# Kernel optimization log

Hardware: AMD Instinct MI355X
Metric: run time of the kernel (lower is better)

The kernel has to match this reference:

```python
import jax, jax.numpy as jnp
from jax import lax
import numpy as np

B, S, T, R = 64, 50, 50, 2   # batch, n_prev_sents, n_words, n_responses
V, H = 32000, 256            # vocab, hidden (= emb_size)


def gru_scan(xs, h0, Wih, Whh, bih, bhh):
    """Torch-style GRU over xs [T, N, I]; returns (outs [T,N,H], h_last [N,H])."""
    gi_all = jnp.einsum('tni,gi->tng', xs, Wih) + bih  # input gates precomputed
    def step(h, gi):
        gh = h @ Whh.T + bhh
        ir, iz, inn = jnp.split(gi, 3, -1)
        hr, hz, hn = jnp.split(gh, 3, -1)
        r = jax.nn.sigmoid(ir + hr)
        z = jax.nn.sigmoid(iz + hz)
        n = jnp.tanh(inn + r * hn)
        h = (1.0 - z) * n + z * h
        return h, h
    h_last, outs = lax.scan(step, h0, gi_all)
    return outs, h_last


def agent_tables():
    # replicates get_agent_emb: np.random.seed(1), one fresh uniform table per batch
    np.random.seed(1)
    return jnp.asarray(np.stack([np.random.uniform(0, 1, (S + 1, H)) for _ in range(B)]).astype(np.float32))


def setup_inputs() -> dict:
    key = jax.random.key(0)
    ks = jax.random.split(key, 24)
    k = 1.0 / np.sqrt(H)
    u = lambda kk, shape: jax.random.uniform(kk, shape, jnp.float32, -k, k)
    inp = {
        'context': jax.random.randint(ks[0], (B, S, T), 0, V, jnp.int32),
        'response': jax.random.randint(ks[1], (B, R, T), 0, V, jnp.int32),
        'spk_agents': jax.random.randint(ks[2], (B, S), 0, S + 1, jnp.int32),
        'emb_utter': jax.random.normal(ks[3], (V, H), jnp.float32) * 0.1,
        'emb_resp': jax.random.normal(ks[4], (V, H), jnp.float32) * 0.1,
        'utter_Wih': u(ks[5], (3 * H, H)), 'utter_Whh': u(ks[6], (3 * H, H)),
        'utter_bih': u(ks[7], (3 * H,)), 'utter_bhh': u(ks[8], (3 * H,)),
        'ctx_Wih': u(ks[9], (3 * H, 2 * H)), 'ctx_Whh': u(ks[10], (3 * H, H)),
        'ctx_bih': u(ks[11], (3 * H,)), 'ctx_bhh': u(ks[12], (3 * H,)),
        'resp_Wih': u(ks[13], (3 * H, H)), 'resp_Whh': u(ks[14], (3 * H, H)),
        'resp_bih': u(ks[15], (3 * H,)), 'resp_bhh': u(ks[16], (3 * H,)),
        'spk_Wih': u(ks[17], (3 * H, H)), 'spk_Whh': u(ks[18], (3 * H, H)),
        'spk_bih': u(ks[19], (3 * H,)), 'spk_bhh': u(ks[20], (3 * H,)),
    }
    return inp


def forward(context, response, spk_agents, emb_utter, emb_resp,
            utter_Wih, utter_Whh, utter_bih, utter_bhh,
            ctx_Wih, ctx_Whh, ctx_bih, ctx_bhh,
            resp_Wih, resp_Whh, resp_bih, resp_bhh,
            spk_Wih, spk_Whh, spk_bih, spk_bhh):
    # ---- utterance encoder: all B*S utterances batched through one GRU ----
    xu = emb_utter[context.reshape(B * S, T)]                 # [B*S, T, H]
    xu = jnp.transpose(xu, (1, 0, 2))                         # [T, B*S, H]
    _, hu = gru_scan(xu, jnp.zeros((B * S, H), jnp.float32),
                     utter_Wih, utter_Whh, utter_bih, utter_bhh)
    utter_hidden = hu.reshape(B, S, H).transpose(1, 0, 2)     # [S, B, H]

    # ---- agent embeddings (per-batch random tables, gathered by speaker id) ----
    tables = agent_tables()                                   # [B, S+1, H] constant
    agent_emb = jnp.take_along_axis(tables, spk_agents[:, :, None].astype(jnp.int32), axis=1)  # [B,S,H]
    agent_emb = jnp.transpose(agent_emb, (1, 0, 2))           # [S, B, H]

    # ---- context GRU over utterances ----
    ctx_in = jnp.concatenate([utter_hidden, agent_emb], axis=2)  # [S, B, 2H]
    context_output, ctx_h = gru_scan(ctx_in, jnp.zeros((B, H), jnp.float32),
                                     ctx_Wih, ctx_Whh, ctx_bih, ctx_bhh)
    context_hidden = ctx_h[None]                              # [1, B, H]

    # ---- speaker encoder: masked GRU == GRU over each speaker's subsequence ----
    sp_ids = jnp.arange(S + 1)
    active = (spk_agents[:, :, None] == sp_ids[None, None, :])  # [B, S, S+1]
    active_t = jnp.transpose(active, (1, 0, 2))                 # [S, B, S+1]
    gi_all = jnp.einsum('sbh,gh->sbg', context_output, spk_Wih) + spk_bih  # [S, B, 3H]

    def spk_step(h, inputs):
        gi, act = inputs                                        # gi [B,3H], act [B,S+1]
        gh = jnp.einsum('bsh,gh->bsg', h, spk_Whh) + spk_bhh    # [B, S+1, 3H]
        ir, iz, inn = jnp.split(gi[:, None, :], 3, -1)
        hr, hz, hn = jnp.split(gh, 3, -1)
        r = jax.nn.sigmoid(ir + hr)
        z = jax.nn.sigmoid(iz + hz)
        n = jnp.tanh(inn + r * hn)
        h_new = (1.0 - z) * n + z * h
        return jnp.where(act[:, :, None], h_new, h), None

    h_spk, _ = lax.scan(spk_step, jnp.zeros((B, S + 1, H), jnp.float32), (gi_all, active_t))
    present = active.any(axis=1)                               # [B, S+1]
    spk_emb = h_spk * present[:, :, None]                      # rows of absent speakers stay 0
    spk_emb_mask = (present & (sp_ids[None, :] > 0)).astype(jnp.float32)  # [B, S+1]

    # ---- response encoder: all B*R responses batched ----
    xr = emb_resp[response.reshape(B * R, T)]                  # [B*R, T, H]
    xr = jnp.transpose(xr, (1, 0, 2))                          # [T, B*R, H]
    outs, hr_ = gru_scan(xr, jnp.zeros((B * R, H), jnp.float32),
                         resp_Wih, resp_Whh, resp_bih, resp_bhh)
    resp_output = outs.reshape(T, B, R, H).transpose(2, 0, 1, 3)  # [R, T, B, H]
    resp_hidden = hr_.reshape(B, R, H).transpose(1, 0, 2)         # [R, B, H]

    return (context_output, context_hidden, resp_output, resp_hidden, spk_emb, spk_emb_mask)


def reference(context, response, spk_agents, emb_utter, emb_resp,
              utter_Wih, utter_Whh, utter_bih, utter_bhh,
              ctx_Wih, ctx_Whh, ctx_bih, ctx_bhh,
              resp_Wih, resp_Whh, resp_bih, resp_bhh,
              spk_Wih, spk_Whh, spk_bih, spk_bhh):
    return forward(context, response, spk_agents, emb_utter, emb_resp,
                   utter_Wih, utter_Whh, utter_bih, utter_bhh,
                   ctx_Wih, ctx_Whh, ctx_bih, ctx_bhh,
                   resp_Wih, resp_Whh, resp_bih, resp_bhh,
                   spk_Wih, spk_Whh, spk_bih, spk_bhh)
```

## Files before the change

kernel.cpp:

```cpp
#include <hip/hip_runtime.h>
#include <hip/hip_bf16.h>
#include <stdint.h>
#include <stdlib.h>
#include <math.h>

typedef __hip_bfloat16 bf16;
typedef unsigned short ushort;
typedef __attribute__((ext_vector_type(8))) short bhalf8;
typedef __attribute__((ext_vector_type(4))) float f32x4;

#define Bn 64
#define Sn 50
#define Tn 50
#define Hn 256

#define OFF_CTX_OUT   0
#define OFF_CTX_HID   819200
#define OFF_RESP_OUT  835584
#define OFF_RESP_HID  2473984
#define OFF_SPK_EMB   2506752
#define OFF_SPK_MASK  3342336

#define WS_FLAG   0u
#define WS_HU     256u
// ... 23 lines not shown
template<bool BF>
__device__ __forceinline__ bhalf8 ldfrag(const void* __restrict__ p, size_t i) {
    if (BF) {
        return *(const bhalf8*)((const ushort*)p + i);
    } else {
        const float* q = (const float*)p + i;
        float4 a = *(const float4*)q;
        float4 b = *(const float4*)(q + 4);
        bhalf8 r;
        r[0] = (short)f2bf(a.x); r[1] = (short)f2bf(a.y);
        r[2] = (short)f2bf(a.z); r[3] = (short)f2bf(a.w);
        r[4] = (short)f2bf(b.x); r[5] = (short)f2bf(b.y);
        r[6] = (short)f2bf(b.z); r[7] = (short)f2bf(b.w);
        return r;
    }
}
template<bool BF>
__device__ __forceinline__ float ldw(const void* __restrict__ p, int i) {
    return BF ? bf2f(((const ushort*)p)[i]) : ((const float*)p)[i];
}
template<bool BF>
__device__ __forceinline__ void stout(void* __restrict__ out, size_t i, float v) {
    if (BF) ((ushort*)out)[i] = f2bf(v);
    else    ((float*)out)[i] = v;
}
__device__ __forceinline__ float fsigm(float x) {
    return __builtin_amdgcn_rcpf(1.f + __expf(-x));
}
__device__ __forceinline__ float ftanh(float x) {
    float e = __expf(-2.f * x);
    return (1.f - e) * __builtin_amdgcn_rcpf(1.f + e);
}

__global__ void sniff_kernel(const void* __restrict__ w, int* __restrict__ flag) {
    const unsigned int* p = (const unsigned int*)w;
    int tid = threadIdx.x;
    bool big = false;
    for (int i = tid; i < 512; i += 64) {
        float v = b2f_bits(p[i] << 16);
        if (!(fabsf(v) <= 1.0f)) big = true;
    }
    unsigned long long m = __ballot(big);
    if (tid == 0) *flag = (m == 0ull) ? 1 : 0;
}


template<bool BF>
__device__ void vocab_utt_body(
    const void* __restrict__ emb_u, const void* __restrict__ uWih,
    const void* __restrict__ ubih,
    char* __restrict__ Q, float* __restrict__ SC,
    float* bhs, float (*rmx)[16])
{
    const int tid = threadIdx.x;
    const int w = tid >> 6, l = tid & 63, quad = l >> 4, c = l & 15;

    for (int i = tid; i < 768; i += 512) bhs[i] = ldw<BF>(ubih, i);

    bhalf8 wf[3][2][8];
    #pragma unroll
    for (int g = 0; g < 3; ++g)
        #pragma unroll
        for (int ctl = 0; ctl < 2; ++ctl) {
            const int gcol = g * 256 + 32 * w + 16 * ctl + c;
            #pragma unroll
            for (int tk = 0; tk < 8; ++tk)
                wf[g][ctl][tk] = ldfrag<BF>(uWih, (size_t)gcol * 256 + 32 * tk + 8 * quad);
        }
    __syncthreads();

    for (int vt = blockIdx.x; vt < 2000; vt += gridDim.x) {
        f32x4 acc[3][2];
        #pragma unroll
        for (int g = 0; g < 3; ++g)
            #pragma unroll
            for (int ctl = 0; ctl < 2; ++ctl) {
                float b = bhs[g * 256 + 32 * w + 16 * ctl + c];
                acc[g][ctl] = (f32x4){b, b, b, b};
            }
        #pragma unroll
        for (int tk = 0; tk < 8; ++tk) {
            bhalf8 a = ldfrag<BF>(emb_u, (size_t)(vt * 16 + c) * 256 + 32 * tk + 8 * quad);
            #pragma unroll
            for (int g = 0; g < 3; ++g)
                #pragma unroll
                for (int ctl = 0; ctl < 2; ++ctl)
                    acc[g][ctl] = __builtin_amdgcn_mfma_f32_16x16x32_bf16(
                        a, wf[g][ctl][tk], acc[g][ctl], 0, 0, 0);
        }

        float mx[4];
        #pragma unroll
        for (int r = 0; r < 4; ++r) {
            float v = 0.f;
            #pragma unroll
            for (int g = 0; g < 3; ++g)
                #pragma unroll
                for (int ctl = 0; ctl < 2; ++ctl)
                    v = fmaxf(v, fabsf(acc[g][ctl][r]));
            mx[r] = v;
        }
        #pragma unroll
        for (int off = 1; off < 16; off <<= 1)
            #pragma unroll
            for (int r = 0; r < 4; ++r)
                mx[r] = fmaxf(mx[r], __shfl_xor(mx[r], off));
        if (c == 0)
            #pragma unroll
            for (int r = 0; r < 4; ++r) rmx[w][4 * quad + r] = mx[r];
        __syncthreads();

        #pragma unroll
        for (int r = 0; r < 4; ++r) {
            const int m = 4 * quad + r;
            float s = fmaxf(fmaxf(fmaxf(rmx[0][m], rmx[1][m]), fmaxf(rmx[2][m], rmx[3][m])),
                            fmaxf(fmaxf(rmx[4][m], rmx[5][m]), fmaxf(rmx[6][m], rmx[7][m])));
            float scale = s * (1.f / 127.f);
            float inv   = (s > 0.f) ? (127.f / s) : 0.f;
            #pragma unroll
            for (int g = 0; g < 3; ++g)
                #pragma unroll
                for (int ctl = 0; ctl < 2; ++ctl) {
                    int qv = __float2int_rn(acc[g][ctl][r] * inv);
                    qv = max(-127, min(127, qv));
                    Q[(size_t)(vt * 16 + m) * 768 + g * 256 + 32 * w + 16 * ctl + c] = (char)qv;
                }
            if (w == 0 && c == 0) SC[vt * 16 + m] = scale;
        }
        __syncthreads();
    }
}

__global__ __launch_bounds__(512, 1) void vocab_utt_kernel(
    const void* emb_u, const void* uWih, const void* ubih,
    char* Q, float* SC, const int* flag)
{
    __shared__ float bhs[768];
    __shared__ float rmx[8][16];
    if (*flag) vocab_utt_body<true >(emb_u, uWih, ubih, Q, SC, bhs, rmx);
    else       vocab_utt_body<false>(emb_u, uWih, ubih, Q, SC, bhs, rmx);
}

template<bool BF>
__device__ void rec_utt_body(
    const int* __restrict__ ctx_tok,
    const char* __restrict__ Q, const float* __restrict__ SC,
    const void* __restrict__ uWhh, const void* __restrict__ ubhh,
    ushort* __restrict__ H_u,
    char (*gq)[16][784], float* gsc_all , ushort (*hb)[16][264])
{
    const int n0 = blockIdx.x * 16;
    const int tid = threadIdx.x;
    const int w = tid >> 6, l = tid & 63, quad = l >> 4, c = l & 15;

    for (int i = tid; i < 16 * 264; i += 512) (&hb[0][0][0])[i] = 0;
    for (int i = tid; i < Tn * 16; i += 512) {
        const int t = i >> 4, m = i & 15;
        gsc_all[i] = SC[ctx_tok[(n0 + m) * Tn + t]];
    }

    float breg[3][2];
    #pragma unroll
    for (int g = 0; g < 3; ++g)
        #pragma unroll
        for (int ctl = 0; ctl < 2; ++ctl)
            breg[g][ctl] = ldw<BF>(ubhh, g * 256 + 32 * w + 16 * ctl + c);

    bhalf8 wf[3][2][8];
    #pragma unroll
    for (int g = 0; g < 3; ++g)
        #pragma unroll
        for (int ctl = 0; ctl < 2; ++ctl) {
            const int gcol = g * 256 + 32 * w + 16 * ctl + c;
            #pragma unroll
            for (int tk = 0; tk < 8; ++tk)
                wf[g][ctl][tk] = ldfrag<BF>(uWhh, (size_t)gcol * 256 + 32 * tk + 8 * quad);
        }

    float st[2][4];
    #pragma unroll
    for (int ctl = 0; ctl < 2; ++ctl)
        #pragma unroll
        for (int r = 0; r < 4; ++r) st[ctl][r] = 0.f;

    #pragma unroll
    for (int k = 0; k < 2; ++k) {
        const int m = 2 * w + k;
        const int tok = ctx_tok[(n0 + m) * Tn + 0];
        if (l < 48)
            gld_lds16(Q + (size_t)tok * 768 + l * 16, &gq[0][m][0]);
    }
    __syncthreads();

    int p = 0;
    for (int t = 0; t < Tn; ++t) {
        if (t < Tn - 1) {
            #pragma unroll
            for (int k = 0; k < 2; ++k) {
                const int m = 2 * w + k;
                const int tok = ctx_tok[(n0 + m) * Tn + t + 1];
                if (l < 48)
                    gld_lds16(Q + (size_t)tok * 768 + l * 16, &gq[p ^ 1][m][0]);
            }
        }

        f32x4 acc[3][2];
        #pragma unroll
        for (int g = 0; g < 3; ++g)
            #pragma unroll
            for (int ctl = 0; ctl < 2; ++ctl) {
                float b = breg[g][ctl];
                acc[g][ctl] = (f32x4){b, b, b, b};
            }
        #pragma unroll
        for (int tk = 0; tk < 8; ++tk) {
            bhalf8 a = *(const bhalf8*)(&hb[p][c][32 * tk + 8 * quad]);
            #pragma unroll
            for (int g = 0; g < 3; ++g)
                #pragma unroll
                for (int ctl = 0; ctl < 2; ++ctl)
                    acc[g][ctl] = __builtin_amdgcn_mfma_f32_16x16x32_bf16(
                        a, wf[g][ctl][tk], acc[g][ctl], 0, 0, 0);
        }

        #pragma unroll
        for (int ctl = 0; ctl < 2; ++ctl) {
            const int u = 32 * w + 16 * ctl + c;
            #pragma unroll
            for (int r = 0; r < 4; ++r) {
                const int m = 4 * quad + r;
                const float s = gsc_all[t * 16 + m];
                float gr = s * (float)(signed char)gq[p][m][u];
                float gz = s * (float)(signed char)gq[p][m][256 + u];
                float gn = s * (float)(signed char)gq[p][m][512 + u];
                float rr = fsigm(gr + acc[0][ctl][r]);
                float zz = fsigm(gz + acc[1][ctl][r]);
                float nn = ftanh(gn + rr * acc[2][ctl][r]);
                float h  = (1.f - zz) * nn + zz * st[ctl][r];
                st[ctl][r] = h;
                hb[p ^ 1][m][u] = f2bf(h);
            }
        }
        __syncthreads();
        p ^= 1;
    }

    #pragma unroll
    for (int ctl = 0; ctl < 2; ++ctl)
        #pragma unroll
        for (int r = 0; r < 4; ++r)
            H_u[(size_t)(n0 + 4 * quad + r) * Hn + 32 * w + 16 * ctl + c] = f2bf(st[ctl][r]);
}

__global__ __launch_bounds__(512, 1) void rec_utt_kernel(
    const int* ctx_tok, const char* Q, const float* SC,
    const void* uWhh, const void* ubhh, ushort* H_u, const int* flag)
{
    __shared__ __align__(16) char   gq[2][16][784];
    __shared__ float  gsc_all[Tn * 16];
    __shared__ __align__(16) ushort hb[2][16][264];
    if (*flag) rec_utt_body<true >(ctx_tok, Q, SC, uWhh, ubhh, H_u, gq, gsc_all, hb);
    else       rec_utt_body<false>(ctx_tok, Q, SC, uWhh, ubhh, H_u, gq, gsc_all, hb);
}

template<bool BF>
__device__ void respgi_body(
    int bid,
    const int* __restrict__ rsp_tok, const void* __restrict__ emb_r,
    const void* __restrict__ rWih, const void* __restrict__ rbih,
    ushort* __restrict__ RG, float* bhs)
{
    const int tid = threadIdx.x;
    const int w = tid >> 6, l = tid & 63, quad = l >> 4, c = l & 15;

    for (int i = tid; i < 768; i += 512) bhs[i] = ldw<BF>(rbih, i);

    bhalf8 wf[3][2][8];
    #pragma unroll
    for (int g = 0; g < 3; ++g)
        #pragma unroll
        for (int ctl = 0; ctl < 2; ++ctl) {
            const int gcol = g * 256 + 32 * w + 16 * ctl + c;
            #pragma unroll
            for (int tk = 0; tk < 8; ++tk)
                wf[g][ctl][tk] = ldfrag<BF>(rWih, (size_t)gcol * 256 + 32 * tk + 8 * quad);
        }
    __syncthreads();

    const int inst = bid * 16 + c;
    const int tok  = rsp_tok[inst];

    f32x4 acc[3][2];
    #pragma unroll
    for (int g = 0; g < 3; ++g)
        #pragma unroll
        for (int ctl = 0; ctl < 2; ++ctl) {
            float b = bhs[g * 256 + 32 * w + 16 * ctl + c];
            acc[g][ctl] = (f32x4){b, b, b, b};
        }
    #pragma unroll
    for (int tk = 0; tk < 8; ++tk) {
        bhalf8 a = ldfrag<BF>(emb_r, (size_t)tok * 256 + 32 * tk + 8 * quad);
        #pragma unroll
        for (int g = 0; g < 3; ++g)
            #pragma unroll
            for (int ctl = 0; ctl < 2; ++ctl)
                acc[g][ctl] = __builtin_amdgcn_mfma_f32_16x16x32_bf16(
                    a, wf[g][ctl][tk], acc[g][ctl], 0, 0, 0);
    }
    #pragma unroll
    for (int g = 0; g < 3; ++g)
        #pragma unroll
        for (int ctl = 0; ctl < 2; ++ctl)
            #pragma unroll
            for (int r = 0; r < 4; ++r)
                RG[(size_t)(bid * 16 + 4 * quad + r) * 768
                   + g * 256 + 32 * w + 16 * ctl + c] = f2bf(acc[g][ctl][r]);
}

template<bool BF>
__device__ void rec_resp_body(
    int bid,
    const ushort* __restrict__ RG,
    const void* __restrict__ rWhh, const void* __restrict__ rbhh,
    void* __restrict__ outp,
    ushort (*gx)[16][776], ushort (*hb)[16][264])
{
    const int n0 = bid * 16;
    const int tid = threadIdx.x;
    const int w = tid >> 6, l = tid & 63, quad = l >> 4, c = l & 15;

    for (int i = tid; i < 16 * 264; i += 512) (&hb[0][0][0])[i] = 0;

    float breg[3][2];
    #pragma unroll
    for (int g = 0; g < 3; ++g)
        #pragma unroll
        for (int ctl = 0; ctl < 2; ++ctl)
            breg[g][ctl] = ldw<BF>(rbhh, g * 256 + 32 * w + 16 * ctl + c);

    bhalf8 wf[3][2][8];
    #pragma unroll
    for (int g = 0; g < 3; ++g)
        #pragma unroll
        for (int ctl = 0; ctl < 2; ++ctl) {
            const int gcol = g * 256 + 32 * w + 16 * ctl + c;
            #pragma unroll
            for (int tk = 0; tk < 8; ++tk)
                wf[g][ctl][tk] = ldfrag<BF>(rWhh, (size_t)gcol * 256 + 32 * tk + 8 * quad);
        }

    float st[2][4];
    #pragma unroll
    for (int ctl = 0; ctl < 2; ++ctl)
        #pragma unroll
        for (int r = 0; r < 4; ++r) st[ctl][r] = 0.f;

    #pragma unroll
    for (int k = 0; k < 2; ++k) {
        const int m = 2 * w + k;
        const ushort* src = RG + (size_t)((n0 + m) * Tn + 0) * 768;
        if (l < 48) {
            gld_lds16(src + l * 8,       &gx[0][m][0]);
            gld_lds16(src + 384 + l * 8, &gx[0][m][384]);
        }
    }
    __syncthreads();

    int p = 0;
    for (int t = 0; t < Tn; ++t) {
        if (t < Tn - 1) {
            #pragma unroll
            for (int k = 0; k < 2; ++k) {
                const int m = 2 * w + k;
                const ushort* src = RG + (size_t)((n0 + m) * Tn + t + 1) * 768;
                if (l < 48) {
                    gld_lds16(src + l * 8,       &gx[p ^ 1][m][0]);
                    gld_lds16(src + 384 + l * 8, &gx[p ^ 1][m][384]);
                }
            }
        }
        if (t > 0) {
            #pragma unroll
            for (int ctl = 0; ctl < 2; ++ctl) {
                const int u = 32 * w + 16 * ctl + c;
                #pragma unroll
                for (int r = 0; r < 4; ++r) {
                    const int n = n0 + 4 * quad + r, bb = n >> 1, ri = n & 1;
                    stout<BF>(outp, OFF_RESP_OUT
                              + (size_t)((ri * Tn + (t - 1)) * Bn + bb) * Hn + u,
                              st[ctl][r]);
                }
            }
        }

        f32x4 acc[3][2];
        #pragma unroll
        for (int g = 0; g < 3; ++g)
            #pragma unroll
            for (int ctl = 0; ctl < 2; ++ctl) {
                float b = breg[g][ctl];
                acc[g][ctl] = (f32x4){b, b, b, b};
            }
        #pragma unroll
        for (int tk = 0; tk < 8; ++tk) {
            bhalf8 a = *(const bhalf8*)(&hb[p][c][32 * tk + 8 * quad]);
            #pragma unroll
            for (int g = 0; g < 3; ++g)
                #pragma unroll
                for (int ctl = 0; ctl < 2; ++ctl)
                    acc[g][ctl] = __builtin_amdgcn_mfma_f32_16x16x32_bf16(
                        a, wf[g][ctl][tk], acc[g][ctl], 0, 0, 0);
        }

        #pragma unroll
        for (int ctl = 0; ctl < 2; ++ctl) {
            const int u = 32 * w + 16 * ctl + c;
            #pragma unroll
            for (int r = 0; r < 4; ++r) {
                const int m = 4 * quad + r;
                float gr = bf2f(gx[p][m][u]);
                float gz = bf2f(gx[p][m][256 + u]);
                float gn = bf2f(gx[p][m][512 + u]);
                float rr = fsigm(gr + acc[0][ctl][r]);
                float zz = fsigm(gz + acc[1][ctl][r]);
                float nn = ftanh(gn + rr * acc[2][ctl][r]);
                float h  = (1.f - zz) * nn + zz * st[ctl][r];
                st[ctl][r] = h;
                hb[p ^ 1][m][u] = f2bf(h);
            }
        }
        __syncthreads();
        p ^= 1;
    }

    #pragma unroll
    for (int ctl = 0; ctl < 2; ++ctl) {
        const int u = 32 * w + 16 * ctl + c;
        #pragma unroll
        for (int r = 0; r < 4; ++r) {
            const int n = n0 + 4 * quad + r, bb = n >> 1, ri = n & 1;
            stout<BF>(outp, OFF_RESP_OUT
                      + (size_t)((ri * Tn + (Tn - 1)) * Bn + bb) * Hn + u, st[ctl][r]);
            stout<BF>(outp, OFF_RESP_HID + (size_t)(ri * Bn + bb) * Hn + u, st[ctl][r]);
        }
    }
}

template<bool BF>
__device__ void gi_ctx_body(
    int bid,
    const ushort* __restrict__ H_u, const ushort* __restrict__ tblbf,
    const int* __restrict__ spk_agents,
    const void* __restrict__ Wih, const void* __restrict__ bih,
    ushort* __restrict__ GIc, float* bhs)
{
    const int tid = threadIdx.x;
    const int w = tid >> 6, l = tid & 63, quad = l >> 4, c = l & 15;

    for (int i = tid; i < 768; i += 512) bhs[i] = ldw<BF>(bih, i);
    __syncthreads();

    const int m0 = bid * 16;
    const int m  = m0 + c, s = m >> 6, b = m & 63;
    const int a  = spk_agents[b * Sn + s];
    const ushort* arow0 = H_u   + (size_t)(b * Sn + s) * Hn;
    const ushort* arow1 = tblbf + (size_t)(b * 51 + a) * Hn;

    f32x4 acc[3][2];
    #pragma unroll
    for (int g = 0; g < 3; ++g)
        #pragma unroll
        for (int ctl = 0; ctl < 2; ++ctl) {
            float bb = bhs[g * 256 + 32 * w + 16 * ctl + c];
            acc[g][ctl] = (f32x4){bb, bb, bb, bb};
        }

    for (int half = 0; half < 2; ++half) {
        const ushort* ar = half ? arow1 : arow0;
        bhalf8 af[8];
        #pragma unroll
        for (int tk = 0; tk < 8; ++tk)
            af[tk] = *(const bhalf8*)(ar + 32 * tk + 8 * quad);
        #pragma unroll
        for (int g = 0; g < 3; ++g) {
            bhalf8 wf[2][8];
            #pragma unroll
            for (int ctl = 0; ctl < 2; ++ctl) {
                const int gcol = g * 256 + 32 * w + 16 * ctl + c;
                #pragma unroll
                for (int tk = 0; tk < 8; ++tk)
                    wf[ctl][tk] = ldfrag<BF>(Wih,
                        (size_t)gcol * 512 + half * 256 + 32 * tk + 8 * quad);
            }
            #pragma unroll
            for (int tk = 0; tk < 8; ++tk)
                #pragma unroll
                for (int ctl = 0; ctl < 2; ++ctl)
                    acc[g][ctl] = __builtin_amdgcn_mfma_f32_16x16x32_bf16(
                        af[tk], wf[ctl][tk], acc[g][ctl], 0, 0, 0);
        }
    }

    #pragma unroll
    for (int g = 0; g < 3; ++g)
        #pragma unroll
        for (int ctl = 0; ctl < 2; ++ctl)
            #pragma unroll
            for (int r = 0; r < 4; ++r)
                GIc[(size_t)(m0 + 4 * quad + r) * 768
                    + g * 256 + 32 * w + 16 * ctl + c] = f2bf(acc[g][ctl][r]);
}

__global__ __launch_bounds__(512, 1) void gates2_kernel(
    const int* rsp_tok, const void* emb_r, const void* rWih, const void* rbih,
    ushort* RG,
    const ushort* H_u, const ushort* tblbf, const int* spk_agents,
    const void* cWih, const void* cbih, ushort* GIc, const int* flag)
{
    __shared__ float bhs[768];
    if (blockIdx.x < 400) {
        if (*flag) respgi_body<true >(blockIdx.x, rsp_tok, emb_r, rWih, rbih, RG, bhs);
        else       respgi_body<false>(blockIdx.x, rsp_tok, emb_r, rWih, rbih, RG, bhs);
    } else {
        const int bid = blockIdx.x - 400;
        if (*flag) gi_ctx_body<true >(bid, H_u, tblbf, spk_agents, cWih, cbih, GIc, bhs);
        else       gi_ctx_body<false>(bid, H_u, tblbf, spk_agents, cWih, cbih, GIc, bhs);
    }
}

template<bool BF>
__device__ void ctx_rec_body(
    int bid,
    const ushort* __restrict__ GIc,
    const void* __restrict__ Whh, const void* __restrict__ bhh,
    float* __restrict__ CO, void* __restrict__ outp,
    ushort (*gx)[16][776], ushort (*hb)[16][264])
{
    const int n0 = bid * 16;
    const int tid = threadIdx.x;
    const int w = tid >> 6, l = tid & 63, quad = l >> 4, c = l & 15;

    for (int i = tid; i < 16 * 264; i += 512) (&hb[0][0][0])[i] = 0;

    float breg[3][2];
    #pragma unroll
    for (int g = 0; g < 3; ++g)
        #pragma unroll
        for (int ctl = 0; ctl < 2; ++ctl)
            breg[g][ctl] = ldw<BF>(bhh, g * 256 + 32 * w + 16 * ctl + c);

    bhalf8 wf[3][2][8];
    #pragma unroll
    for (int g = 0; g < 3; ++g)
        #pragma unroll
        for (int ctl = 0; ctl < 2; ++ctl) {
            const int gcol = g * 256 + 32 * w + 16 * ctl + c;
            #pragma unroll
            for (int tk = 0; tk < 8; ++tk)
                wf[g][ctl][tk] = ldfrag<BF>(Whh, (size_t)gcol * 256 + 32 * tk + 8 * quad);
        }

    float st[2][4];
    #pragma unroll
    for (int ctl = 0; ctl < 2; ++ctl)
        #pragma unroll
        for (int r = 0; r < 4; ++r) st[ctl][r] = 0.f;

    #pragma unroll
    for (int k = 0; k < 2; ++k) {
        const int m = 2 * w + k;
        const ushort* src = GIc + (size_t)(0 * Bn + n0 + m) * 768;
        if (l < 48) {
            gld_lds16(src + l * 8,       &gx[0][m][0]);
            gld_lds16(src + 384 + l * 8, &gx[0][m][384]);
        }
    }
    __syncthreads();

    int p = 0;
    for (int t = 0; t < Sn; ++t) {
        if (t < Sn - 1) {
            #pragma unroll
            for (int k = 0; k < 2; ++k) {
                const int m = 2 * w + k;
                const ushort* src = GIc + (size_t)((t + 1) * Bn + n0 + m) * 768;
                if (l < 48) {
                    gld_lds16(src + l * 8,       &gx[p ^ 1][m][0]);
                    gld_lds16(src + 384 + l * 8, &gx[p ^ 1][m][384]);
                }
            }
        }
        if (t > 0) {
            #pragma unroll
            for (int ctl = 0; ctl < 2; ++ctl) {
                const int u = 32 * w + 16 * ctl + c;
                #pragma unroll
                for (int r = 0; r < 4; ++r) {
                    const size_t gri = (size_t)((t - 1) * Bn + n0 + 4 * quad + r);
                    CO[gri * Hn + u] = st[ctl][r];
                    stout<BF>(outp, OFF_CTX_OUT + gri * Hn + u, st[ctl][r]);
                }
            }
        }

        f32x4 acc[3][2];
        #pragma unroll
        for (int g = 0; g < 3; ++g)
            #pragma unroll
            for (int ctl = 0; ctl < 2; ++ctl) {
                float b = breg[g][ctl];
                acc[g][ctl] = (f32x4){b, b, b, b};
            }
        #pragma unroll
        for (int tk = 0; tk < 8; ++tk) {
            bhalf8 a = *(const bhalf8*)(&hb[p][c][32 * tk + 8 * quad]);
            #pragma unroll
            for (int g = 0; g < 3; ++g)
                #pragma unroll
                for (int ctl = 0; ctl < 2; ++ctl)
                    acc[g][ctl] = __builtin_amdgcn_mfma_f32_16x16x32_bf16(
                        a, wf[g][ctl][tk], acc[g][ctl], 0, 0, 0);
        }

        #pragma unroll
        for (int ctl = 0; ctl < 2; ++ctl) {
            const int u = 32 * w + 16 * ctl + c;
            #pragma unroll
            for (int r = 0; r < 4; ++r) {
                const int m = 4 * quad + r;
                float gr = bf2f(gx[p][m][u]);
                float gz = bf2f(gx[p][m][256 + u]);
                float gn = bf2f(gx[p][m][512 + u]);
                float rr = fsigm(gr + acc[0][ctl][r]);
                float zz = fsigm(gz + acc[1][ctl][r]);
                float nn = ftanh(gn + rr * acc[2][ctl][r]);
                float h  = (1.f - zz) * nn + zz * st[ctl][r];
                st[ctl][r] = h;
                hb[p ^ 1][m][u] = f2bf(h);
            }
        }
        __syncthreads();
        p ^= 1;
    }

    #pragma unroll
    for (int ctl = 0; ctl < 2; ++ctl) {
        const int u = 32 * w + 16 * ctl + c;
        #pragma unroll
        for (int r = 0; r < 4; ++r) {
            const int m = 4 * quad + r;
            const size_t gri = (size_t)((Sn - 1) * Bn + n0 + m);
            CO[gri * Hn + u] = st[ctl][r];
            stout<BF>(outp, OFF_CTX_OUT + gri * Hn + u, st[ctl][r]);
            stout<BF>(outp, OFF_CTX_HID + (size_t)(n0 + m) * Hn + u, st[ctl][r]);
        }
    }
}

__global__ __launch_bounds__(512, 1) void rec2_kernel(
    const ushort* GIc, const void* cWhh, const void* cbhh, float* CO,
    const ushort* RG, const void* rWhh, const void* rbhh,
    void* outp, const int* flag)
{
    __shared__ __align__(16) ushort gx[2][16][776];
    __shared__ __align__(16) ushort hb[2][16][264];
    if (blockIdx.x < 4) {
        if (*flag) ctx_rec_body<true >(blockIdx.x, GIc, cWhh, cbhh, CO, outp, gx, hb);
        else       ctx_rec_body<false>(blockIdx.x, GIc, cWhh, cbhh, CO, outp, gx, hb);
    } else {
        const int bid = blockIdx.x - 4;
        if (*flag) rec_resp_body<true >(bid, RG, rWhh, rbhh, outp, gx, hb);
        else       rec_resp_body<false>(bid, RG, rWhh, rbhh, outp, gx, hb);
    }
}

template<bool BF>
__device__ void gi_spk_body(
    const float* __restrict__ CO,
    const void* __restrict__ Wih, const void* __restrict__ bih,
    ushort* __restrict__ GIs, float* bhs)
{
    const int tid = threadIdx.x;
    const int w = tid >> 6, l = tid & 63, quad = l >> 4, c = l & 15;

    for (int i = tid; i < 768; i += 512) bhs[i] = ldw<BF>(bih, i);

    bhalf8 wf[3][2][8];
    #pragma unroll
    for (int g = 0; g < 3; ++g)
        #pragma unroll
        for (int ctl = 0; ctl < 2; ++ctl) {
            const int gcol = g * 256 + 32 * w + 16 * ctl + c;
            #pragma unroll
            for (int tk = 0; tk < 8; ++tk)
                wf[g][ctl][tk] = ldfrag<BF>(Wih, (size_t)gcol * 256 + 32 * tk + 8 * quad);
        }
    __syncthreads();

    f32x4 acc[3][2];
    #pragma unroll
    for (int g = 0; g < 3; ++g)
        #pragma unroll
        for (int ctl = 0; ctl < 2; ++ctl) {
            float b = bhs[g * 256 + 32 * w + 16 * ctl + c];
            acc[g][ctl] = (f32x4){b, b, b, b};
        }
    #pragma unroll
    for (int tk = 0; tk < 8; ++tk) {
        bhalf8 a = ldfrag<false>(CO, (size_t)(blockIdx.x * 16 + c) * 256 + 32 * tk + 8 * quad);
        #pragma unroll
        for (int g = 0; g < 3; ++g)
            #pragma unroll
            for (int ctl = 0; ctl < 2; ++ctl)
                acc[g][ctl] = __builtin_amdgcn_mfma_f32_16x16x32_bf16(
                    a, wf[g][ctl][tk], acc[g][ctl], 0, 0, 0);
    }
    #pragma unroll
    for (int g = 0; g < 3; ++g)
        #pragma unroll
        for (int ctl = 0; ctl < 2; ++ctl)
            #pragma unroll
            for (int r = 0; r < 4; ++r)
                GIs[(size_t)(blockIdx.x * 16 + 4 * quad + r) * 768
                    + g * 256 + 32 * w + 16 * ctl + c] = f2bf(acc[g][ctl][r]);
}

__global__ __launch_bounds__(512, 1) void gi_spk_kernel(
    const float* CO, const void* Wih, const void* bih, ushort* GIs, const int* flag)
{
    __shared__ float bhs[768];
    if (*flag) gi_spk_body<true >(CO, Wih, bih, GIs, bhs);
    else       gi_spk_body<false>(CO, Wih, bih, GIs, bhs);
}

#define SSTR 264
template<bool BF>
__device__ void spk_rec_body(
    const ushort* __restrict__ GIs,
    const void* __restrict__ Whh, const void* __restrict__ bhh,
    const int* __restrict__ spk_agents,
    void* __restrict__ outp,
    ushort* S , ushort (*gx)[4][776], int* pres , float* bhs)
{
    const int b0 = blockIdx.x * 4;
    const int tid = threadIdx.x;
    const int w = tid >> 6, l = tid & 63, quad = l >> 4, c = l & 15;

    for (int i = tid; i < 768; i += 512) bhs[i] = ldw<BF>(bhh, i);
    for (int i = tid; i < 4 * 51 * SSTR; i += 512) S[i] = 0;
    for (int i = tid; i < 4 * 51; i += 512) pres[i] = 0;

    bhalf8 wf[3][2][8];
    #pragma unroll
    for (int g = 0; g < 3; ++g)
        #pragma unroll
        for (int ctl = 0; ctl < 2; ++ctl) {
            const int gcol = g * 256 + 32 * w + 16 * ctl + c;
            #pragma unroll
            for (int tk = 0; tk < 8; ++tk)
                wf[g][ctl][tk] = ldfrag<BF>(Whh, (size_t)gcol * 256 + 32 * tk + 8 * quad);
        }

    {
        const int row = w >> 1, ch = w & 1;
        const ushort* src = GIs + (size_t)(0 * Bn + b0 + row) * 768 + ch * 384;
        if (l < 48) gld_lds16(src + l * 8, &gx[0][row][ch * 384]);
    }
    __syncthreads();

    int p = 0;
    for (int t = 0; t < Sn; ++t) {
        const int va = (c < 4) ? spk_agents[(b0 + c) * Sn + t] : 0;
        const int mb = (c < 4) ? c : 0;

        if (t < Sn - 1) {
            const int row = w >> 1, ch = w & 1;
            const ushort* src = GIs + (size_t)((t + 1) * Bn + b0 + row) * 768 + ch * 384;
            if (l < 48) gld_lds16(src + l * 8, &gx[p ^ 1][row][ch * 384]);
        }

        f32x4 acc[3][2];
        #pragma unroll
        for (int g = 0; g < 3; ++g)
            #pragma unroll
            for (int ctl = 0; ctl < 2; ++ctl) {
                float b = bhs[g * 256 + 32 * w + 16 * ctl + c];
                acc[g][ctl] = (f32x4){b, b, b, b};
            }
        const ushort* srow = &S[(mb * 51 + va) * SSTR];
        #pragma unroll
        for (int tk = 0; tk < 8; ++tk) {
            bhalf8 a = *(const bhalf8*)(srow + 32 * tk + 8 * quad);
            #pragma unroll
            for (int g = 0; g < 3; ++g)
                #pragma unroll
                for (int ctl = 0; ctl < 2; ++ctl)
                    acc[g][ctl] = __builtin_amdgcn_mfma_f32_16x16x32_bf16(
                        a, wf[g][ctl][tk], acc[g][ctl], 0, 0, 0);
        }
        __syncthreads();

        if (quad == 0) {
            int vv[4];
            #pragma unroll
            for (int r = 0; r < 4; ++r) vv[r] = spk_agents[(b0 + r) * Sn + t];
            #pragma unroll
            for (int ctl = 0; ctl < 2; ++ctl) {
                const int u = 32 * w + 16 * ctl + c;
                #pragma unroll
                for (int r = 0; r < 4; ++r) {
                    ushort* sp = &S[(r * 51 + vv[r]) * SSTR + u];
                    float gr = bf2f(gx[p][r][u]);
                    float gz = bf2f(gx[p][r][256 + u]);
                    float gn = bf2f(gx[p][r][512 + u]);
                    float hprev = bf2f(*sp);
                    float rr = fsigm(gr + acc[0][ctl][r]);
                    float zz = fsigm(gz + acc[1][ctl][r]);
                    float nn = ftanh(gn + rr * acc[2][ctl][r]);
                    float h  = (1.f - zz) * nn + zz * hprev;
                    *sp = f2bf(h);
                }
            }
        }
        if (tid < 4) pres[tid * 51 + spk_agents[(b0 + tid) * Sn + t]] = 1;
        __syncthreads();
        p ^= 1;
    }
    __syncthreads();

    for (int idx = tid; idx < 4 * 51 * 256; idx += 512) {
        const int mb2 = idx / (51 * 256);
        const int rem = idx - mb2 * (51 * 256);
        const int v = rem >> 8, u = rem & 255;
        float val = bf2f(S[(mb2 * 51 + v) * SSTR + u]);
        stout<BF>(outp, OFF_SPK_EMB + (size_t)((b0 + mb2) * 51 + v) * Hn + u, val);
    }
    for (int idx = tid; idx < 4 * 51; idx += 512) {
        const int mb2 = idx / 51, v = idx - mb2 * 51;
        stout<BF>(outp, OFF_SPK_MASK + (size_t)((b0 + mb2) * 51 + v),
                  (pres[mb2 * 51 + v] && v > 0) ? 1.f : 0.f);
    }
}

__global__ __launch_bounds__(512, 1) void spk_rec_kernel(
    const ushort* GIs, const void* Whh, const void* bhh,
    const int* spk_agents, void* outp, const int* flag)
{
    __shared__ __align__(16) ushort S[4 * 51 * SSTR];
    __shared__ __align__(16) ushort gx[2][4][776];
    __shared__ int    pres[4 * 51];
    __shared__ float  bhs[768];
    if (*flag) spk_rec_body<true >(GIs, Whh, bhh, spk_agents, outp, S, gx, pres, bhs);
    else       spk_rec_body<false>(GIs, Whh, bhh, spk_agents, outp, S, gx, pres, bhs);
}

namespace {
inline uint16_t host_f2bf(float f) {
    union { float f; uint32_t u; } c; c.f = f;
    return (uint16_t)((c.u + 0x7fffu + ((c.u >> 16) & 1u)) >> 16);
}
struct MT19937 {
    uint32_t mt[624]; int mti;
    void seed(uint32_t s) {
        mt[0] = s;
        for (int i = 1; i < 624; ++i)
            mt[i] = 1812433253u * (mt[i - 1] ^ (mt[i - 1] >> 30)) + (uint32_t)i;
        mti = 624;
    }
    uint32_t next() {
        if (mti >= 624) {
            for (int i = 0; i < 624; ++i) {
                uint32_t y = (mt[i] & 0x80000000u) | (mt[(i + 1) % 624] & 0x7fffffffu);
                mt[i] = mt[(i + 397) % 624] ^ (y >> 1) ^ ((y & 1u) ? 0x9908b0dfu : 0u);
            }
            mti = 0;
        }
        uint32_t y = mt[mti++];
        y ^= y >> 11; y ^= (y << 7) & 0x9d2c5680u; y ^= (y << 15) & 0xefc60000u; y ^= y >> 18;
        return y;
    }
    double rd() {
        uint32_t a = next() >> 5, b = next() >> 6;
        return (a * 67108864.0 + b) / 9007199254740992.0;
    }
};

uint16_t* get_host_tables() {
    static uint16_t* p = [] {
        void* q = nullptr;
        if (hipHostMalloc(&q, 835584 * sizeof(uint16_t), hipHostMallocDefault) != hipSuccess)
            q = malloc(835584 * sizeof(uint16_t));
        uint16_t* h = (uint16_t*)q;
        MT19937 g; g.seed(1u);
        for (int i = 0; i < 835584; ++i)
            h[i] = host_f2bf((float)g.rd());
        return h;
    }();
    return p;
}
}

extern "C" void kernel_launch(void* const* d_in, const int* in_sizes, int n_in,
                              void* d_out, int out_size, void* d_ws, size_t ws_size,
                              hipStream_t stream)
{
    const int* ctx_tok    = (const int*)d_in[0];
    const int* rsp_tok    = (const int*)d_in[1];
    const int* spk_agents = (const int*)d_in[2];
    const void* emb_u = d_in[3];
    const void* emb_r = d_in[4];
    const void* uWih = d_in[5],  *uWhh = d_in[6],  *ubih = d_in[7],  *ubhh = d_in[8];
    const void* cWih = d_in[9],  *cWhh = d_in[10], *cbih = d_in[11], *cbhh = d_in[12];
    const void* rWih = d_in[13], *rWhh = d_in[14], *rbih = d_in[15], *rbhh = d_in[16];
    const void* sWih = d_in[17], *sWhh = d_in[18], *sbih = d_in[19], *sbhh = d_in[20];
    (void)in_sizes; (void)n_in; (void)out_size; (void)ws_size;

    char* ws  = (char*)d_ws;
    char* reg = ws + WS_REG;
    int*      flag = (int*)(ws + WS_FLAG);
    ushort*   H_u  = (ushort*)(ws + WS_HU);
    char*     UQ   = (char*)(reg + RG_UTTQ);
    float*    USC  = (float*)(reg + RG_UTTSC);
    ushort*   RG   = (ushort*)(reg + RG_RESPGI);
    float*    CO   = (float*)(reg + RG_CO);
    ushort*   GIc  = (ushort*)(reg + RG_GIC);
    ushort*   GIs  = (ushort*)(reg + RG_GIS);
    ushort*   tbl  = (ushort*)(reg + RG_TBL);
    void*     out  = d_out;

    sniff_kernel<<<1, 64, 0, stream>>>(uWih, flag);

    vocab_utt_kernel<<<250, 512, 0, stream>>>(emb_u, uWih, ubih, UQ, USC, flag);
    rec_utt_kernel<<<200, 512, 0, stream>>>(ctx_tok, UQ, USC, uWhh, ubhh, H_u, flag);

    hipMemcpyAsync(tbl, get_host_tables(), 835584 * sizeof(uint16_t),
                   hipMemcpyHostToDevice, stream);

    gates2_kernel<<<600, 512, 0, stream>>>(rsp_tok, emb_r, rWih, rbih, RG,
                                           H_u, tbl, spk_agents, cWih, cbih, GIc, flag);

    rec2_kernel<<<12, 512, 0, stream>>>(GIc, cWhh, cbhh, CO,
                                        RG, rWhh, rbhh, out, flag);

    gi_spk_kernel<<<200, 512, 0, stream>>>(CO, sWih, sbih, GIs, flag);
    spk_rec_kernel<<<16, 512, 0, stream>>>(GIs, sWhh, sbhh, spk_agents, out, flag);
}
```

Baseline: 1.236 ms.

## Double waves per block in GRU recurrence kernels to halve per-wave column work

The utterance, context and response recurrence kernels now launch 1024 threads (16 waves) instead of 512, and each wave owns 16 hidden columns instead of 32. Per-wave work per timestep drops from 48 to 24 MFMAs, and the weight fragments held in registers are halved. The aim is to shorten the serial per-step latency of the recurrence by spreading it across more waves. The cost is more waves contending at each per-step __syncthreads, and tighter register limits per thread at 1024 threads per block.

```diff
diff --git a/kernel.cpp b/kernel.cpp
--- a/kernel.cpp
+++ b/kernel.cpp
@@ -199,107 +199,82 @@
     const int n0 = blockIdx.x * 16;
     const int tid = threadIdx.x;
     const int w = tid >> 6, l = tid & 63, quad = l >> 4, c = l & 15;
-
-    for (int i = tid; i < 16 * 264; i += 512) (&hb[0][0][0])[i] = 0;
-    for (int i = tid; i < Tn * 16; i += 512) {
+    const int u = 16 * w + c;
+
+    for (int i = tid; i < 16 * 264; i += 1024) (&hb[0][0][0])[i] = 0;
+    for (int i = tid; i < Tn * 16; i += 1024) {
         const int t = i >> 4, m = i & 15;
         gsc_all[i] = SC[ctx_tok[(n0 + m) * Tn + t]];
     }
 
-    float breg[3][2];
-    #pragma unroll
-    for (int g = 0; g < 3; ++g)
-        #pragma unroll
-        for (int ctl = 0; ctl < 2; ++ctl)
-            breg[g][ctl] = ldw<BF>(ubhh, g * 256 + 32 * w + 16 * ctl + c);
-
-    bhalf8 wf[3][2][8];
-    #pragma unroll
-    for (int g = 0; g < 3; ++g)
-        #pragma unroll
-        for (int ctl = 0; ctl < 2; ++ctl) {
-            const int gcol = g * 256 + 32 * w + 16 * ctl + c;
-            #pragma unroll
-            for (int tk = 0; tk < 8; ++tk)
-                wf[g][ctl][tk] = ldfrag<BF>(uWhh, (size_t)gcol * 256 + 32 * tk + 8 * quad);
-        }
-
-    float st[2][4];
-    #pragma unroll
-    for (int ctl = 0; ctl < 2; ++ctl)
-        #pragma unroll
-        for (int r = 0; r < 4; ++r) st[ctl][r] = 0.f;
-
-    #pragma unroll
-    for (int k = 0; k < 2; ++k) {
-        const int m = 2 * w + k;
-        const int tok = ctx_tok[(n0 + m) * Tn + 0];
-        if (l < 48)
-            gld_lds16(Q + (size_t)tok * 768 + l * 16, &gq[0][m][0]);
+    float breg[3];
+    #pragma unroll
+    for (int g = 0; g < 3; ++g)
+        breg[g] = ldw<BF>(ubhh, g * 256 + u);
+
+    bhalf8 wf[3][8];
+    #pragma unroll
+    for (int g = 0; g < 3; ++g)
+        #pragma unroll
+        for (int tk = 0; tk < 8; ++tk)
+            wf[g][tk] = ldfrag<BF>(uWhh, (size_t)(g * 256 + u) * 256 + 32 * tk + 8 * quad);
+
+    float st[4];
+    #pragma unroll
+    for (int r = 0; r < 4; ++r) st[r] = 0.f;
+
+    {
+        const int tok = ctx_tok[(n0 + w) * Tn + 0];
+        if (l < 48) gld_lds16(Q + (size_t)tok * 768 + l * 16, &gq[0][w][0]);
     }
     __syncthreads();
 
     int p = 0;
     for (int t = 0; t < Tn; ++t) {
         if (t < Tn - 1) {
-            #pragma unroll
-            for (int k = 0; k < 2; ++k) {
-                const int m = 2 * w + k;
-                const int tok = ctx_tok[(n0 + m) * Tn + t + 1];
-                if (l < 48)
-                    gld_lds16(Q + (size_t)tok * 768 + l * 16, &gq[p ^ 1][m][0]);
-            }
-        }
-
-        f32x4 acc[3][2];
-        #pragma unroll
-        for (int g = 0; g < 3; ++g)
-            #pragma unroll
-            for (int ctl = 0; ctl < 2; ++ctl) {
-                float b = breg[g][ctl];
-                acc[g][ctl] = (f32x4){b, b, b, b};
-            }
+            const int tok = ctx_tok[(n0 + w) * Tn + t + 1];
+            if (l < 48) gld_lds16(Q + (size_t)tok * 768 + l * 16, &gq[p ^ 1][w][0]);
+        }
+
+        f32x4 acc[3];
+        #pragma unroll
+        for (int g = 0; g < 3; ++g) {
+            float b = breg[g];
+            acc[g] = (f32x4){b, b, b, b};
+        }
         #pragma unroll
         for (int tk = 0; tk < 8; ++tk) {
             bhalf8 a = *(const bhalf8*)(&hb[p][c][32 * tk + 8 * quad]);
             #pragma unroll
             for (int g = 0; g < 3; ++g)
-                #pragma unroll
-                for (int ctl = 0; ctl < 2; ++ctl)
-                    acc[g][ctl] = __builtin_amdgcn_mfma_f32_16x16x32_bf16(
-                        a, wf[g][ctl][tk], acc[g][ctl], 0, 0, 0);
-        }
-
-        #pragma unroll
-        for (int ctl = 0; ctl < 2; ++ctl) {
-            const int u = 32 * w + 16 * ctl + c;
-            #pragma unroll
-            for (int r = 0; r < 4; ++r) {
-                const int m = 4 * quad + r;
-                const float s = gsc_all[t * 16 + m];
-                float gr = s * (float)(signed char)gq[p][m][u];
-                float gz = s * (float)(signed char)gq[p][m][256 + u];
-                float gn = s * (float)(signed char)gq[p][m][512 + u];
-                float rr = fsigm(gr + acc[0][ctl][r]);
-                float zz = fsigm(gz + acc[1][ctl][r]);
-                float nn = ftanh(gn + rr * acc[2][ctl][r]);
-                float h  = (1.f - zz) * nn + zz * st[ctl][r];
-                st[ctl][r] = h;
-                hb[p ^ 1][m][u] = f2bf(h);
-            }
+                acc[g] = __builtin_amdgcn_mfma_f32_16x16x32_bf16(
+                    a, wf[g][tk], acc[g], 0, 0, 0);
+        }
+
+        #pragma unroll
+        for (int r = 0; r < 4; ++r) {
+            const int m = 4 * quad + r;
+            const float s = gsc_all[t * 16 + m];
+            float gr = s * (float)(signed char)gq[p][m][u];
+            float gz = s * (float)(signed char)gq[p][m][256 + u];
+            float gn = s * (float)(signed char)gq[p][m][512 + u];
+            float rr = fsigm(gr + acc[0][r]);
+            float zz = fsigm(gz + acc[1][r]);
+            float nn = ftanh(gn + rr * acc[2][r]);
+            float h  = (1.f - zz) * nn + zz * st[r];
+            st[r] = h;
+            hb[p ^ 1][m][u] = f2bf(h);
         }
         __syncthreads();
         p ^= 1;
     }
 
     #pragma unroll
-    for (int ctl = 0; ctl < 2; ++ctl)
-        #pragma unroll
-        for (int r = 0; r < 4; ++r)
-            H_u[(size_t)(n0 + 4 * quad + r) * Hn + 32 * w + 16 * ctl + c] = f2bf(st[ctl][r]);
-}
-
-__global__ __launch_bounds__(512, 1) void rec_utt_kernel(
+    for (int r = 0; r < 4; ++r)
+        H_u[(size_t)(n0 + 4 * quad + r) * Hn + u] = f2bf(st[r]);
+}
+
+__global__ __launch_bounds__(1024, 1) void rec_utt_kernel(
     const int* ctx_tok, const char* Q, const float* SC,
     const void* uWhh, const void* ubhh, ushort* H_u, const int* flag)
 {
@@ -376,40 +351,31 @@
     const int n0 = bid * 16;
     const int tid = threadIdx.x;
     const int w = tid >> 6, l = tid & 63, quad = l >> 4, c = l & 15;
-
-    for (int i = tid; i < 16 * 264; i += 512) (&hb[0][0][0])[i] = 0;
-
-    float breg[3][2];
-    #pragma unroll
-    for (int g = 0; g < 3; ++g)
-        #pragma unroll
-        for (int ctl = 0; ctl < 2; ++ctl)
-            breg[g][ctl] = ldw<BF>(rbhh, g * 256 + 32 * w + 16 * ctl + c);
-
-    bhalf8 wf[3][2][8];
-    #pragma unroll
-    for (int g = 0; g < 3; ++g)
-        #pragma unroll
-        for (int ctl = 0; ctl < 2; ++ctl) {
-            const int gcol = g * 256 + 32 * w + 16 * ctl + c;
-            #pragma unroll
-            for (int tk = 0; tk < 8; ++tk)
-                wf[g][ctl][tk] = ldfrag<BF>(rWhh, (size_t)gcol * 256 + 32 * tk + 8 * quad);
-        }
-
-    float st[2][4];
-    #pragma unroll
-    for (int ctl = 0; ctl < 2; ++ctl)
-        #pragma unroll
-        for (int r = 0; r < 4; ++r) st[ctl][r] = 0.f;
-
-    #pragma unroll
-    for (int k = 0; k < 2; ++k) {
-        const int m = 2 * w + k;
-        const ushort* src = RG + (size_t)((n0 + m) * Tn + 0) * 768;
+    const int u = 16 * w + c;
+
+    for (int i = tid; i < 16 * 264; i += 1024) (&hb[0][0][0])[i] = 0;
+
+    float breg[3];
+    #pragma unroll
+    for (int g = 0; g < 3; ++g)
+        breg[g] = ldw<BF>(rbhh, g * 256 + u);
+
+    bhalf8 wf[3][8];
+    #pragma unroll
+    for (int g = 0; g < 3; ++g)
+        #pragma unroll
+        for (int tk = 0; tk < 8; ++tk)
+            wf[g][tk] = ldfrag<BF>(rWhh, (size_t)(g * 256 + u) * 256 + 32 * tk + 8 * quad);
+
+    float st[4];
+    #pragma unroll
+    for (int r = 0; r < 4; ++r) st[r] = 0.f;
+
+    {
+        const ushort* src = RG + (size_t)((n0 + w) * Tn + 0) * 768;
         if (l < 48) {
-            gld_lds16(src + l * 8,       &gx[0][m][0]);
-            gld_lds16(src + 384 + l * 8, &gx[0][m][384]);
+            gld_lds16(src + l * 8,       &gx[0][w][0]);
+            gld_lds16(src + 384 + l * 8, &gx[0][w][384]);
         }
     }
     __syncthreads();
@@ -417,80 +383,59 @@
     int p = 0;
     for (int t = 0; t < Tn; ++t) {
         if (t < Tn - 1) {
-            #pragma unroll
-            for (int k = 0; k < 2; ++k) {
-                const int m = 2 * w + k;
-                const ushort* src = RG + (size_t)((n0 + m) * Tn + t + 1) * 768;
-                if (l < 48) {
-                    gld_lds16(src + l * 8,       &gx[p ^ 1][m][0]);
-                    gld_lds16(src + 384 + l * 8, &gx[p ^ 1][m][384]);
-                }
+            const ushort* src = RG + (size_t)((n0 + w) * Tn + t + 1) * 768;
+            if (l < 48) {
+                gld_lds16(src + l * 8,       &gx[p ^ 1][w][0]);
+                gld_lds16(src + 384 + l * 8, &gx[p ^ 1][w][384]);
             }
         }
         if (t > 0) {
             #pragma unroll
-            for (int ctl = 0; ctl < 2; ++ctl) {
-                const int u = 32 * w + 16 * ctl + c;
-                #pragma unroll
-                for (int r = 0; r < 4; ++r) {
-                    const int n = n0 + 4 * quad + r, bb = n >> 1, ri = n & 1;
-                    stout<BF>(outp, OFF_RESP_OUT
-                              + (size_t)((ri * Tn + (t - 1)) * Bn + bb) * Hn + u,
-                              st[ctl][r]);
-                }
+            for (int r = 0; r < 4; ++r) {
+                const int n = n0 + 4 * quad + r, bb = n >> 1, ri = n & 1;
+                stout<BF>(outp, OFF_RESP_OUT
+                          + (size_t)((ri * Tn + (t - 1)) * Bn + bb) * Hn + u, st[r]);
             }
         }
 
-        f32x4 acc[3][2];
-        #pragma unroll
-        for (int g = 0; g < 3; ++g)
-            #pragma unroll
-            for (int ctl = 0; ctl < 2; ++ctl) {
-                float b = breg[g][ctl];
-                acc[g][ctl] = (f32x4){b, b, b, b};
-            }
+        f32x4 acc[3];
+        #pragma unroll
+        for (int g = 0; g < 3; ++g) {
+            float b = breg[g];
+            acc[g] = (f32x4){b, b, b, b};
+        }
         #pragma unroll
         for (int tk = 0; tk < 8; ++tk) {
             bhalf8 a = *(const bhalf8*)(&hb[p][c][32 * tk + 8 * quad]);
             #pragma unroll
             for (int g = 0; g < 3; ++g)
-                #pragma unroll
-                for (int ctl = 0; ctl < 2; ++ctl)
-                    acc[g][ctl] = __builtin_amdgcn_mfma_f32_16x16x32_bf16(
-                        a, wf[g][ctl][tk], acc[g][ctl], 0, 0, 0);
-        }
-
-        #pragma unroll
-        for (int ctl = 0; ctl < 2; ++ctl) {
-            const int u = 32 * w + 16 * ctl + c;
-            #pragma unroll
-            for (int r = 0; r < 4; ++r) {
-                const int m = 4 * quad + r;
-                float gr = bf2f(gx[p][m][u]);
-                float gz = bf2f(gx[p][m][256 + u]);
-                float gn = bf2f(gx[p][m][512 + u]);
-                float rr = fsigm(gr + acc[0][ctl][r]);
-                float zz = fsigm(gz + acc[1][ctl][r]);
-                float nn = ftanh(gn + rr * acc[2][ctl][r]);
-                float h  = (1.f - zz) * nn + zz * st[ctl][r];
-                st[ctl][r] = h;
-                hb[p ^ 1][m][u] = f2bf(h);
-            }
+                acc[g] = __builtin_amdgcn_mfma_f32_16x16x32_bf16(
+                    a, wf[g][tk], acc[g], 0, 0, 0);
+        }
+
+        #pragma unroll
+        for (int r = 0; r < 4; ++r) {
+            const int m = 4 * quad + r;
+            float gr = bf2f(gx[p][m][u]);
+            float gz = bf2f(gx[p][m][256 + u]);
+            float gn = bf2f(gx[p][m][512 + u]);
+            float rr = fsigm(gr + acc[0][r]);
+            float zz = fsigm(gz + acc[1][r]);
+            float nn = ftanh(gn + rr * acc[2][r]);
+            float h  = (1.f - zz) * nn + zz * st[r];
+            st[r] = h;
+            hb[p ^ 1][m][u] = f2bf(h);
         }
         __syncthreads();
         p ^= 1;
     }
 
     #pragma unroll
-    for (int ctl = 0; ctl < 2; ++ctl) {
-        const int u = 32 * w + 16 * ctl + c;
-        #pragma unroll
-        for (int r = 0; r < 4; ++r) {
-            const int n = n0 + 4 * quad + r, bb = n >> 1, ri = n & 1;
-            stout<BF>(outp, OFF_RESP_OUT
-                      + (size_t)((ri * Tn + (Tn - 1)) * Bn + bb) * Hn + u, st[ctl][r]);
-            stout<BF>(outp, OFF_RESP_HID + (size_t)(ri * Bn + bb) * Hn + u, st[ctl][r]);
-        }
+    for (int r = 0; r < 4; ++r) {
+        const int n = n0 + 4 * quad + r, bb = n >> 1, ri = n & 1;
+        stout<BF>(outp, OFF_RESP_OUT
+                  + (size_t)((ri * Tn + (Tn - 1)) * Bn + bb) * Hn + u, st[r]);
+        stout<BF>(outp, OFF_RESP_HID + (size_t)(ri * Bn + bb) * Hn + u, st[r]);
     }
 }
 
@@ -587,40 +532,31 @@
     const int n0 = bid * 16;
     const int tid = threadIdx.x;
     const int w = tid >> 6, l = tid & 63, quad = l >> 4, c = l & 15;
-
-    for (int i = tid; i < 16 * 264; i += 512) (&hb[0][0][0])[i] = 0;
-
-    float breg[3][2];
-    #pragma unroll
-    for (int g = 0; g < 3; ++g)
-        #pragma unroll
-        for (int ctl = 0; ctl < 2; ++ctl)
-            breg[g][ctl] = ldw<BF>(bhh, g * 256 + 32 * w + 16 * ctl + c);
-
-    bhalf8 wf[3][2][8];
-    #pragma unroll
-    for (int g = 0; g < 3; ++g)
-        #pragma unroll
-        for (int ctl = 0; ctl < 2; ++ctl) {
-            const int gcol = g * 256 + 32 * w + 16 * ctl + c;
-            #pragma unroll
-            for (int tk = 0; tk < 8; ++tk)
-                wf[g][ctl][tk] = ldfrag<BF>(Whh, (size_t)gcol * 256 + 32 * tk + 8 * quad);
-        }
-
-    float st[2][4];
-    #pragma unroll
-    for (int ctl = 0; ctl < 2; ++ctl)
-        #pragma unroll
-        for (int r = 0; r < 4; ++r) st[ctl][r] = 0.f;
-
-    #pragma unroll
-    for (int k = 0; k < 2; ++k) {
-        const int m = 2 * w + k;
-        const ushort* src = GIc + (size_t)(0 * Bn + n0 + m) * 768;
+    const int u = 16 * w + c;
+
+    for (int i = tid; i < 16 * 264; i += 1024) (&hb[0][0][0])[i] = 0;
+
+    float breg[3];
+    #pragma unroll
+    for (int g = 0; g < 3; ++g)
+        breg[g] = ldw<BF>(bhh, g * 256 + u);
+
+    bhalf8 wf[3][8];
+    #pragma unroll
+    for (int g = 0; g < 3; ++g)
+        #pragma unroll
+        for (int tk = 0; tk < 8; ++tk)
+            wf[g][tk] = ldfrag<BF>(Whh, (size_t)(g * 256 + u) * 256 + 32 * tk + 8 * quad);
+
+    float st[4];
+    #pragma unroll
+    for (int r = 0; r < 4; ++r) st[r] = 0.f;
+
+    {
+        const ushort* src = GIc + (size_t)(0 * Bn + n0 + w) * 768;
         if (l < 48) {
-            gld_lds16(src + l * 8,       &gx[0][m][0]);
-            gld_lds16(src + 384 + l * 8, &gx[0][m][384]);
+            gld_lds16(src + l * 8,       &gx[0][w][0]);
+            gld_lds16(src + 384 + l * 8, &gx[0][w][384]);
         }
     }
     __syncthreads();
@@ -628,84 +564,64 @@
     int p = 0;
     for (int t = 0; t < Sn; ++t) {
         if (t < Sn - 1) {
-            #pragma unroll
-            for (int k = 0; k < 2; ++k) {
-                const int m = 2 * w + k;
-                const ushort* src = GIc + (size_t)((t + 1) * Bn + n0 + m) * 768;
-                if (l < 48) {
-                    gld_lds16(src + l * 8,       &gx[p ^ 1][m][0]);
-                    gld_lds16(src + 384 + l * 8, &gx[p ^ 1][m][384]);
-                }
+            const ushort* src = GIc + (size_t)((t + 1) * Bn + n0 + w) * 768;
+            if (l < 48) {
+                gld_lds16(src + l * 8,       &gx[p ^ 1][w][0]);
+                gld_lds16(src + 384 + l * 8, &gx[p ^ 1][w][384]);
             }
         }
         if (t > 0) {
             #pragma unroll
-            for (int ctl = 0; ctl < 2; ++ctl) {
-                const int u = 32 * w + 16 * ctl + c;
-                #pragma unroll
-                for (int r = 0; r < 4; ++r) {
-                    const size_t gri = (size_t)((t - 1) * Bn + n0 + 4 * quad + r);
-                    CO[gri * Hn + u] = st[ctl][r];
-                    stout<BF>(outp, OFF_CTX_OUT + gri * Hn + u, st[ctl][r]);
-                }
+            for (int r = 0; r < 4; ++r) {
+                const size_t gri = (size_t)((t - 1) * Bn + n0 + 4 * quad + r);
+                CO[gri * Hn + u] = st[r];
+                stout<BF>(outp, OFF_CTX_OUT + gri * Hn + u, st[r]);
             }
         }
 
-        f32x4 acc[3][2];
-        #pragma unroll
-        for (int g = 0; g < 3; ++g)
-            #pragma unroll
-            for (int ctl = 0; ctl < 2; ++ctl) {
-                float b = breg[g][ctl];
-                acc[g][ctl] = (f32x4){b, b, b, b};
-            }
+        f32x4 acc[3];
+        #pragma unroll
+        for (int g = 0; g < 3; ++g) {
+            float b = breg[g];
+            acc[g] = (f32x4){b, b, b, b};
+        }
         #pragma unroll
         for (int tk = 0; tk < 8; ++tk) {
             bhalf8 a = *(const bhalf8*)(&hb[p][c][32 * tk + 8 * quad]);
             #pragma unroll
             for (int g = 0; g < 3; ++g)
-                #pragma unroll
-                for (int ctl = 0; ctl < 2; ++ctl)
-                    acc[g][ctl] = __builtin_amdgcn_mfma_f32_16x16x32_bf16(
-                        a, wf[g][ctl][tk], acc[g][ctl], 0, 0, 0);
-        }
-
-        #pragma unroll
-        for (int ctl = 0; ctl < 2; ++ctl) {
-            const int u = 32 * w + 16 * ctl + c;
-            #pragma unroll
-            for (int r = 0; r < 4; ++r) {
-                const int m = 4 * quad + r;
-                float gr = bf2f(gx[p][m][u]);
-                float gz = bf2f(gx[p][m][256 + u]);
-                float gn = bf2f(gx[p][m][512 + u]);
-                float rr = fsigm(gr + acc[0][ctl][r]);
-                float zz = fsigm(gz + acc[1][ctl][r]);
-                float nn = ftanh(gn + rr * acc[2][ctl][r]);
-                float h  = (1.f - zz) * nn + zz * st[ctl][r];
-                st[ctl][r] = h;
-                hb[p ^ 1][m][u] = f2bf(h);
-            }
+                acc[g] = __builtin_amdgcn_mfma_f32_16x16x32_bf16(
+                    a, wf[g][tk], acc[g], 0, 0, 0);
+        }
+
+        #pragma unroll
+        for (int r = 0; r < 4; ++r) {
+            const int m = 4 * quad + r;
+            float gr = bf2f(gx[p][m][u]);
+            float gz = bf2f(gx[p][m][256 + u]);
+            float gn = bf2f(gx[p][m][512 + u]);
+            float rr = fsigm(gr + acc[0][r]);
+            float zz = fsigm(gz + acc[1][r]);
+            float nn = ftanh(gn + rr * acc[2][r]);
+            float h  = (1.f - zz) * nn + zz * st[r];
+            st[r] = h;
+            hb[p ^ 1][m][u] = f2bf(h);
         }
         __syncthreads();
         p ^= 1;
     }
 
     #pragma unroll
-    for (int ctl = 0; ctl < 2; ++ctl) {
-        const int u = 32 * w + 16 * ctl + c;
-        #pragma unroll
-        for (int r = 0; r < 4; ++r) {
-            const int m = 4 * quad + r;
-            const size_t gri = (size_t)((Sn - 1) * Bn + n0 + m);
-            CO[gri * Hn + u] = st[ctl][r];
-            stout<BF>(outp, OFF_CTX_OUT + gri * Hn + u, st[ctl][r]);
-            stout<BF>(outp, OFF_CTX_HID + (size_t)(n0 + m) * Hn + u, st[ctl][r]);
-        }
-    }
-}
-
-__global__ __launch_bounds__(512, 1) void rec2_kernel(
+    for (int r = 0; r < 4; ++r) {
+        const int m = 4 * quad + r;
+        const size_t gri = (size_t)((Sn - 1) * Bn + n0 + m);
+        CO[gri * Hn + u] = st[r];
+        stout<BF>(outp, OFF_CTX_OUT + gri * Hn + u, st[r]);
+        stout<BF>(outp, OFF_CTX_HID + (size_t)(n0 + m) * Hn + u, st[r]);
+    }
+}
+
+__global__ __launch_bounds__(1024, 1) void rec2_kernel(
     const ushort* GIc, const void* cWhh, const void* cbhh, float* CO,
     const ushort* RG, const void* rWhh, const void* rbhh,
     void* outp, const int* flag)
@@ -979,7 +895,7 @@
     sniff_kernel<<<1, 64, 0, stream>>>(uWih, flag);
 
     vocab_utt_kernel<<<250, 512, 0, stream>>>(emb_u, uWih, ubih, UQ, USC, flag);
-    rec_utt_kernel<<<200, 512, 0, stream>>>(ctx_tok, UQ, USC, uWhh, ubhh, H_u, flag);
+    rec_utt_kernel<<<200, 1024, 0, stream>>>(ctx_tok, UQ, USC, uWhh, ubhh, H_u, flag);
 
     hipMemcpyAsync(tbl, get_host_tables(), 835584 * sizeof(uint16_t),
                    hipMemcpyHostToDevice, stream);
@@ -987,8 +903,8 @@
     gates2_kernel<<<600, 512, 0, stream>>>(rsp_tok, emb_r, rWih, rbih, RG,
                                            H_u, tbl, spk_agents, cWih, cbih, GIc, flag);
 
-    rec2_kernel<<<12, 512, 0, stream>>>(GIc, cWhh, cbhh, CO,
-                                        RG, rWhh, rbhh, out, flag);
+    rec2_kernel<<<12, 1024, 0, stream>>>(GIc, cWhh, cbhh, CO,
+                                         RG, rWhh, rbhh, out, flag);
 
     gi_spk_kernel<<<200, 512, 0, stream>>>(CO, sWih, sbih, GIs, flag);
     spk_rec_kernel<<<16, 512, 0, stream>>>(GIs, sWhh, sbhh, spk_agents, out, flag);
```

Result: slower. 1.306 ms (+5.7%).
